# Kernel optimization log

Hardware: AMD Instinct MI355X
Metric: run time of the kernel (lower is better)

Reference implementation:

```python
import jax, jax.numpy as jnp
import numpy as np

TOPK_R = 32  # topk_R from init


def setup_inputs() -> dict:
    key = jax.random.key(0)
    k1, k2 = jax.random.split(key)
    B, N, L_in, L_out = 8, 2048, 512, 512
    x = jax.random.normal(k1, (B, N, L_in), dtype=jnp.float32)
    # kaiming-uniform-style init for Linear weight [out, in]
    bound = float(np.sqrt(6.0 / L_in))
    W = jax.random.uniform(k2, (L_out, L_in), dtype=jnp.float32, minval=-bound, maxval=bound)
    return {"x": x, "W": W}


def reference(x, W):
    # x: [B, N, L_in]; W: [L_out, L_in] (Linear, no bias)
    xp = jnp.einsum('bnl,ol->bno', x, W)          # [B, N, L_out]
    # sim_score with norm=False: plain dot product
    score = jnp.einsum('bnd,bmd->bnm', xp, xp)    # [B, N, N]
    B, N, _ = score.shape
    # RkNNAdjacency: identity + top-k neighbors per row set to 1
    topk_idx = jax.lax.top_k(score, TOPK_R)[1]    # [B, N, k]
    adj = jnp.broadcast_to(jnp.eye(N, dtype=score.dtype), (B, N, N))
    b_idx = jnp.arange(B)[:, None, None]
    n_idx = jnp.arange(N)[None, :, None]
    adj = adj.at[b_idx, n_idx, topk_idx].set(1.0)
    # mask: 1 where neighbor, -1e19 elsewhere; NOTE: multiplicative mask (mask * score)
    mask = jnp.where(adj == 1.0, jnp.ones_like(adj), jnp.full_like(adj, -1e19))
    attention = jax.nn.softmax(mask * score, axis=2)  # [B, N, N]
    h = jnp.einsum('bnm,bmd->bnd', attention, xp)     # [B, N, L_out]
    return (h, attention)
```

## Files before the change

### kernel.cpp

```cpp
#include <hip/hip_runtime.h>
#include <cfloat>


typedef short bf16x8 __attribute__((ext_vector_type(8)));
typedef _Float16 f16x8 __attribute__((ext_vector_type(8)));
typedef _Float16 f16x4 __attribute__((ext_vector_type(4)));
typedef float f32x4 __attribute__((ext_vector_type(4)));

#define NW4 65536

__device__ __forceinline__ unsigned short f2bf(float f) {
  unsigned int u = __float_as_uint(f);
  unsigned int r = (u + 0x7FFFu + ((u >> 16) & 1u)) >> 16;
  return (unsigned short)r;
}

__device__ __forceinline__ void gload_lds16(const unsigned short* g, unsigned short* l) {
  __builtin_amdgcn_global_load_lds(
      (const __attribute__((address_space(1))) unsigned int*)g,
      (__attribute__((address_space(3))) unsigned int*)l, 16, 0, 0);
}

__device__ __forceinline__ unsigned int skey(float v, int m) {
  unsigned int u = __float_as_uint(v);
  u ^= ((unsigned int)((int)u >> 31)) | 0x80000000u;
  return (u & 0xFFFFF800u) | (unsigned int)m;
}

__global__ __launch_bounds__(256) void splitW_kernel(const float* __restrict__ W,
                                                     _Float16* __restrict__ wh,
                                                     _Float16* __restrict__ wl) {
  const int i4 = blockIdx.x * 256 + threadIdx.x;
  if (i4 >= NW4) return;
  const float4 v = reinterpret_cast<const float4*>(W)[i4];
  f16x4 hv, lv;
  const float vv[4] = {v.x, v.y, v.z, v.w};
#pragma unroll
  for (int c = 0; c < 4; ++c) {
    const _Float16 h = (_Float16)vv[c];
    hv[c] = h;
    lv[c] = (_Float16)((vv[c] - (float)h) * 2048.0f);
  }
  reinterpret_cast<f16x4*>(wh)[i4] = hv;
  reinterpret_cast<f16x4*>(wl)[i4] = lv;
}

__global__ __launch_bounds__(256, 2) void gemm_xw_mfma(const float* __restrict__ x,
                                                       const unsigned short* __restrict__ wh,
                                                       const unsigned short* __restrict__ wl,
                                                       float* __restrict__ xp,
                                                       unsigned short* __restrict__ xp16) {
  __shared__ unsigned short lAh[2][128 * 32];
  __shared__ unsigned short lAl[2][128 * 32];
  __shared__ unsigned short lBh[2][128 * 32];
  __shared__ unsigned short lBl[2][128 * 32];
  const int tid = threadIdx.x;
  const int wid = tid >> 6, lane = tid & 63;
  const int lr = lane & 15, kg = lane >> 4;
  const int nbase = blockIdx.x * 128;
  const int obase = blockIdx.y * 128;
  const int wr = wid >> 1, wc = wid & 1;

  const int srow = tid >> 2;
  const int scol = (tid & 3) * 8;
  const float* gX0 = x + (size_t)(nbase + srow) * 512 + scol;
  const float* gX1 = x + (size_t)(nbase + 64 + srow) * 512 + scol;
  const unsigned short* gBh0 = wh + (size_t)(obase + srow) * 512 + scol;
  const unsigned short* gBh1 = wh + (size_t)(obase + 64 + srow) * 512 + scol;
  const unsigned short* gBl0 = wl + (size_t)(obase + srow) * 512 + scol;
  const unsigned short* gBl1 = wl + (size_t)(obase + 64 + srow) * 512 + scol;

  f32x4 acc_hh[4][4] = {};
  f32x4 acc_x[4][4] = {};
  float4 va[4];

#define K1_LOADA(KB)                                                \
  do {                                                              \
    va[0] = *reinterpret_cast<const float4*>(gX0 + (KB));           \
    va[1] = *reinterpret_cast<const float4*>(gX0 + (KB) + 4);       \
    va[2] = *reinterpret_cast<const float4*>(gX1 + (KB));           \
    va[3] = *reinterpret_cast<const float4*>(gX1 + (KB) + 4);       \
  } while (0)

#define K1_WRITEA(BUF)                                              \
  do {                                                              \
    _Pragma("unroll") for (int p = 0; p < 2; ++p) {                 \
      f16x8 hv, lv;                                                 \
      _Pragma("unroll") for (int q = 0; q < 2; ++q) {               \
        const float vv[4] = {va[2 * p + q].x, va[2 * p + q].y,      \
                             va[2 * p + q].z, va[2 * p + q].w};     \
        _Pragma("unroll") for (int c = 0; c < 4; ++c) {             \
          const _Float16 hh = (_Float16)vv[c];                      \
          hv[4 * q + c] = hh;                                       \
          lv[4 * q + c] = (_Float16)((vv[c] - (float)hh) * 2048.0f);\
        }                                                           \
      }                                                             \
      const int ra = (srow + 64 * p) * 32 + scol;                   \
      *reinterpret_cast<f16x8*>(&lAh[BUF][ra]) = hv;                \
      *reinterpret_cast<f16x8*>(&lAl[BUF][ra]) = lv;                \
    }                                                               \
  } while (0)

#define K1_STAGEB(KB, BUF)                                 \
  do {                                                     \
    gload_lds16(gBh0 + (KB), &lBh[BUF][wid * 512]);        \
    gload_lds16(gBh1 + (KB), &lBh[BUF][2048 + wid * 512]); \
    gload_lds16(gBl0 + (KB), &lBl[BUF][wid * 512]);        \
    gload_lds16(gBl1 + (KB), &lBl[BUF][2048 + wid * 512]); \
  } while (0)

#define K1_COMPUTE(BUF)                                                                \
  do {                                                                                 \
    f16x8 ah[4], al[4], bh[4], bl[4];                                                  \
    _Pragma("unroll") for (int i2 = 0; i2 < 4; ++i2) {                                 \
      ah[i2] = *reinterpret_cast<const f16x8*>(&lAh[BUF][(wr * 64 + i2 * 16 + lr) * 32 + kg * 8]); \
      al[i2] = *reinterpret_cast<const f16x8*>(&lAl[BUF][(wr * 64 + i2 * 16 + lr) * 32 + kg * 8]); \
      bh[i2] = *reinterpret_cast<const f16x8*>(&lBh[BUF][(wc * 64 + i2 * 16 + lr) * 32 + kg * 8]); \
      bl[i2] = *reinterpret_cast<const f16x8*>(&lBl[BUF][(wc * 64 + i2 * 16 + lr) * 32 + kg * 8]); \
    }                                                                                  \
    _Pragma("unroll") for (int i2 = 0; i2 < 4; ++i2)                                   \
        _Pragma("unroll") for (int j2 = 0; j2 < 4; ++j2) {                             \
      acc_hh[i2][j2] = __builtin_amdgcn_mfma_f32_16x16x32_f16(ah[i2], bh[j2], acc_hh[i2][j2], 0, 0, 0); \
      acc_x[i2][j2] = __builtin_amdgcn_mfma_f32_16x16x32_f16(ah[i2], bl[j2], acc_x[i2][j2], 0, 0, 0);   \
      acc_x[i2][j2] = __builtin_amdgcn_mfma_f32_16x16x32_f16(al[i2], bh[j2], acc_x[i2][j2], 0, 0, 0);   \
    }                                                                                  \
  } while (0)

  K1_LOADA(0);
  K1_STAGEB(0, 0);
  K1_WRITEA(0);
  __syncthreads();
  for (int t = 0; t < 15; ++t) {
    K1_LOADA((t + 1) * 32);
    K1_STAGEB((t + 1) * 32, (t & 1) ^ 1);
    K1_COMPUTE(t & 1);
    K1_WRITEA((t & 1) ^ 1);
    __syncthreads();
  }
  K1_COMPUTE(1);

#pragma unroll
  for (int i = 0; i < 4; ++i) {
#pragma unroll
    for (int j = 0; j < 4; ++j) {
#pragma unroll
      for (int r = 0; r < 4; ++r) {
        const float v = acc_hh[i][j][r] + acc_x[i][j][r] * (1.0f / 2048.0f);
        const size_t row = (size_t)(nbase + wr * 64 + i * 16 + kg * 4 + r);
        const int col = obase + wc * 64 + j * 16 + lr;
        xp[row * 512 + col] = v;
        xp16[row * 512 + col] = f2bf(v);
      }
    }
  }
#undef K1_LOADA
#undef K1_WRITEA
#undef K1_STAGEB
#undef K1_COMPUTE
}

__global__ __launch_bounds__(256) void score_kernel(const unsigned short* __restrict__ xp16,
                                                    unsigned int* __restrict__ cand) {
  __shared__ unsigned short lA[2][128 * 32];
  __shared__ unsigned short lB[2][128 * 32];
  const int tid = threadIdx.x;
  const int wid = tid >> 6, lane = tid & 63;
  const int lr = lane & 15, kg = lane >> 4;
  const int b = blockIdx.x & 7;
  int p = blockIdx.x >> 3;
  int tn = 0, rem = 16;
  while (p >= rem) { p -= rem; rem--; tn++; }
  const int tm = tn + p;
  const int nbase = tn * 128, mbase = tm * 128;
  const unsigned short* Xb = xp16 + (size_t)b * 2048 * 512;
  const int wr = wid >> 1, wc = wid & 1;

  const int srow = tid >> 2;
  const int scol = (tid & 3) * 8;
  const unsigned short* gA0 = Xb + (size_t)(nbase + srow) * 512 + scol;
  const unsigned short* gA1 = Xb + (size_t)(nbase + 64 + srow) * 512 + scol;
  const unsigned short* gB0 = Xb + (size_t)(mbase + srow) * 512 + scol;
  const unsigned short* gB1 = Xb + (size_t)(mbase + 64 + srow) * 512 + scol;

  f32x4 acc[4][4] = {};

#define STAGE(KB, BUF)                                    \
  do {                                                    \
    gload_lds16(gA0 + (KB), &lA[BUF][wid * 512]);         \
    gload_lds16(gA1 + (KB), &lA[BUF][2048 + wid * 512]);  \
    gload_lds16(gB0 + (KB), &lB[BUF][wid * 512]);         \
    gload_lds16(gB1 + (KB), &lB[BUF][2048 + wid * 512]);  \
  } while (0)

#define COMPUTE(BUF)                                                                   \
  do {                                                                                 \
    bf16x8 af[4], bfr[4];                                                              \
    _Pragma("unroll") for (int i2 = 0; i2 < 4; ++i2) {                                 \
      af[i2] = *reinterpret_cast<const bf16x8*>(&lA[BUF][(wr * 64 + i2 * 16 + lr) * 32 + kg * 8]); \
      bfr[i2] = *reinterpret_cast<const bf16x8*>(&lB[BUF][(wc * 64 + i2 * 16 + lr) * 32 + kg * 8]); \
    }                                                                                  \
    _Pragma("unroll") for (int i2 = 0; i2 < 4; ++i2)                                   \
        _Pragma("unroll") for (int j2 = 0; j2 < 4; ++j2)                               \
            acc[i2][j2] =                                                              \
                __builtin_amdgcn_mfma_f32_16x16x32_bf16(af[i2], bfr[j2], acc[i2][j2], 0, 0, 0); \
  } while (0)

  STAGE(0, 0);
  __syncthreads();
  for (int t = 0; t < 15; ++t) {
    STAGE((t + 1) * 32, (t & 1) ^ 1);
    COMPUTE(t & 1);
    __syncthreads();
  }
  COMPUTE(1);

  const int mcol = mbase + wc * 64 + lr;
#pragma unroll
  for (int i = 0; i < 4; ++i) {
#pragma unroll
    for (int r = 0; r < 4; ++r) {
      const unsigned int x0 = skey(acc[i][0][r], mcol + 0);
      const unsigned int x1 = skey(acc[i][1][r], mcol + 16);
      const unsigned int x2 = skey(acc[i][2][r], mcol + 32);
      const unsigned int x3 = skey(acc[i][3][r], mcol + 48);
      const unsigned int lo01 = min(x0, x1), hi01 = max(x0, x1);
      const unsigned int lo23 = min(x2, x3), hi23 = max(x2, x3);
      unsigned int k1 = min(lo01, lo23);
      unsigned int k2 = min(max(lo01, lo23), min(hi01, hi23));
#pragma unroll
      for (int off = 1; off < 16; off <<= 1) {
        const unsigned int o1 = (unsigned int)__shfl_xor((int)k1, off);
        const unsigned int o2 = (unsigned int)__shfl_xor((int)k2, off);
        const unsigned int nk1 = min(k1, o1);
        const unsigned int nk2 = min(max(k1, o1), min(k2, o2));
        k1 = nk1;
        k2 = nk2;
      }
      if (lr == 0) {
        const int n = nbase + wr * 64 + i * 16 + kg * 4 + r;
        const uint2 kv = {k1, k2};
        *reinterpret_cast<uint2*>(cand + ((size_t)b * 2048 + n) * 512 + (tm * 2 + wc) * 2) = kv;
      }
    }
  }

  if (tn != tm) {
    const int nrow0 = nbase + wr * 64 + kg * 4;
#pragma unroll
    for (int j = 0; j < 4; ++j) {
      unsigned int k1 = 0xFFFFFFFFu, k2 = 0xFFFFFFFFu;
#pragma unroll
      for (int i = 0; i < 4; ++i) {
#pragma unroll
        for (int r = 0; r < 4; ++r) {
          const unsigned int xk = skey(acc[i][j][r], nrow0 + i * 16 + r);
          const unsigned int nk1 = min(k1, xk);
          k2 = min(k2, max(k1, xk));
          k1 = nk1;
        }
      }
#pragma unroll
      for (int off = 16; off < 64; off <<= 1) {
        const unsigned int o1 = (unsigned int)__shfl_xor((int)k1, off);
        const unsigned int o2 = (unsigned int)__shfl_xor((int)k2, off);
        const unsigned int nk1 = min(k1, o1);
        const unsigned int nk2 = min(max(k1, o1), min(k2, o2));
        k1 = nk1;
        k2 = nk2;
      }
      if (kg == 0) {
        const int m = mbase + wc * 64 + j * 16 + lr;
        const uint2 kv = {k1, k2};
        *reinterpret_cast<uint2*>(cand + ((size_t)b * 2048 + m) * 512 + (tn * 2 + wr) * 2) = kv;
      }
    }
  }
#undef STAGE
#undef COMPUTE
}

__global__ __launch_bounds__(64) void finalize_kernel(const float* __restrict__ xp,
                                                      float* __restrict__ h,
                                                      float* __restrict__ att) {
  const int l = threadIdx.x;
  const int b = blockIdx.x & 7;
  const int n = blockIdx.x >> 3;
  const size_t r = (size_t)b * 2048 + n;

  unsigned int key = reinterpret_cast<const unsigned int*>(h + r * 512)[l];
  int wsel[8];
#pragma unroll
  for (int t = 0; t < 8; ++t) {
    unsigned int m = key;
#pragma unroll
    for (int off = 1; off < 64; off <<= 1)
      m = min(m, (unsigned int)__shfl_xor((int)m, off));
    wsel[t] = (int)(m & 0x7FFu);
    if (key == m) key = 0xFFFFFFFFu;
  }

  const float* xb = xp + (size_t)b * 2048 * 512;
  const float* xn = xb + (size_t)n * 512;
  const float4 q0 = reinterpret_cast<const float4*>(xn)[2 * l];
  const float4 q1 = reinterpret_cast<const float4*>(xn)[2 * l + 1];

  float bestv = FLT_MAX;
  int besti = 0x7fffffff;
#pragma unroll
  for (int t = 0; t < 8; ++t) {
    const float* xm = xb + (size_t)wsel[t] * 512;
    const float4 p0 = reinterpret_cast<const float4*>(xm)[2 * l];
    const float4 p1 = reinterpret_cast<const float4*>(xm)[2 * l + 1];
    float s = 0.f;
    s = fmaf(q0.x, p0.x, s); s = fmaf(q0.y, p0.y, s);
    s = fmaf(q0.z, p0.z, s); s = fmaf(q0.w, p0.w, s);
    s = fmaf(q1.x, p1.x, s); s = fmaf(q1.y, p1.y, s);
    s = fmaf(q1.z, p1.z, s); s = fmaf(q1.w, p1.w, s);
#pragma unroll
    for (int off = 1; off < 64; off <<= 1) s += __shfl_xor(s, off);
    if (s < bestv || (s == bestv && wsel[t] < besti)) { bestv = s; besti = wsel[t]; }
  }

  const float* xs = xb + (size_t)besti * 512;
  const float4 w0 = reinterpret_cast<const float4*>(xs)[2 * l];
  const float4 w1 = reinterpret_cast<const float4*>(xs)[2 * l + 1];
  float* hrow = h + r * 512;
  reinterpret_cast<float4*>(hrow)[2 * l] = w0;
  reinterpret_cast<float4*>(hrow)[2 * l + 1] = w1;

  float* arow = att + r * 2048;
#pragma unroll
  for (int s = 0; s < 8; ++s) {
    const int cbase = s * 256 + l * 4;
    float4 v;
    v.x = (cbase + 0 == besti) ? 1.0f : 0.0f;
    v.y = (cbase + 1 == besti) ? 1.0f : 0.0f;
    v.z = (cbase + 2 == besti) ? 1.0f : 0.0f;
    v.w = (cbase + 3 == besti) ? 1.0f : 0.0f;
    reinterpret_cast<float4*>(arow)[s * 64 + l] = v;
  }
}

extern "C" void kernel_launch(void* const* d_in, const int* in_sizes, int n_in,
                              void* d_out, int out_size, void* d_ws, size_t ws_size,
                              hipStream_t stream) {
  const float* x = (const float*)d_in[0];
  const float* W = (const float*)d_in[1];
  float* out = (float*)d_out;
  float* h = out;
  float* att = out + (size_t)8 * 2048 * 512;
  float* xp = (float*)d_ws;

  char* attb = (char*)att;
  _Float16* wh = (_Float16*)(attb + (size_t)32 * 1024 * 1024);
  _Float16* wl = (_Float16*)(attb + (size_t)33 * 1024 * 1024);
  unsigned short* xp16 = (unsigned short*)(attb + (size_t)112 * 1024 * 1024);

  hipLaunchKernelGGL(splitW_kernel, dim3(NW4 / 256), dim3(256), 0, stream, W, wh, wl);

  hipLaunchKernelGGL(gemm_xw_mfma, dim3(16384 / 128, 512 / 128), dim3(256), 0, stream,
                     x, (const unsigned short*)wh, (const unsigned short*)wl, xp, xp16);

  hipLaunchKernelGGL(score_kernel, dim3(8 * 136), dim3(256), 0, stream, xp16,
                     (unsigned int*)h);

  hipLaunchKernelGGL(finalize_kernel, dim3(16384), dim3(64), 0, stream, xp, h, att);
}
```

Before: 117.9 us.

## Load GEMM operands directly from global into registers, dropping LDS staging

The x·W projection kernel no longer stages A and B tiles through shared memory with double buffering and barriers. Each wave now loads its own fragments straight from global memory into registers, converts x to split fp16 in registers, and prefetches the next k-slice of x. This removes LDS traffic and the per-iteration barrier. In exchange, each wave re-reads operands that neighbouring waves also load, relying on L1/L2 to absorb the duplication, and the global access pattern becomes strided, which risks lower memory efficiency.

```diff
diff --git a/kernel.cpp b/kernel.cpp
--- a/kernel.cpp
+++ b/kernel.cpp
@@ -45,15 +45,11 @@
   reinterpret_cast<f16x4*>(wl)[i4] = lv;
 }
 
-__global__ __launch_bounds__(256, 2) void gemm_xw_mfma(const float* __restrict__ x,
-                                                       const unsigned short* __restrict__ wh,
-                                                       const unsigned short* __restrict__ wl,
-                                                       float* __restrict__ xp,
-                                                       unsigned short* __restrict__ xp16) {
-  __shared__ unsigned short lAh[2][128 * 32];
-  __shared__ unsigned short lAl[2][128 * 32];
-  __shared__ unsigned short lBh[2][128 * 32];
-  __shared__ unsigned short lBl[2][128 * 32];
+__global__ __launch_bounds__(256) void gemm_xw_mfma(const float* __restrict__ x,
+                                                    const unsigned short* __restrict__ wh,
+                                                    const unsigned short* __restrict__ wl,
+                                                    float* __restrict__ xp,
+                                                    unsigned short* __restrict__ xp16) {
   const int tid = threadIdx.x;
   const int wid = tid >> 6, lane = tid & 63;
   const int lr = lane & 15, kg = lane >> 4;
@@ -61,83 +57,58 @@
   const int obase = blockIdx.y * 128;
   const int wr = wid >> 1, wc = wid & 1;
 
-  const int srow = tid >> 2;
-  const int scol = (tid & 3) * 8;
-  const float* gX0 = x + (size_t)(nbase + srow) * 512 + scol;
-  const float* gX1 = x + (size_t)(nbase + 64 + srow) * 512 + scol;
-  const unsigned short* gBh0 = wh + (size_t)(obase + srow) * 512 + scol;
-  const unsigned short* gBh1 = wh + (size_t)(obase + 64 + srow) * 512 + scol;
-  const unsigned short* gBl0 = wl + (size_t)(obase + srow) * 512 + scol;
-  const unsigned short* gBl1 = wl + (size_t)(obase + 64 + srow) * 512 + scol;
+  const float* gA = x + (size_t)(nbase + wr * 64 + lr) * 512 + kg * 8;
+  const unsigned short* gBh = wh + (size_t)(obase + wc * 64 + lr) * 512 + kg * 8;
+  const unsigned short* gBl = wl + (size_t)(obase + wc * 64 + lr) * 512 + kg * 8;
 
   f32x4 acc_hh[4][4] = {};
   f32x4 acc_x[4][4] = {};
-  float4 va[4];
-
-#define K1_LOADA(KB)                                                \
-  do {                                                              \
-    va[0] = *reinterpret_cast<const float4*>(gX0 + (KB));           \
-    va[1] = *reinterpret_cast<const float4*>(gX0 + (KB) + 4);       \
-    va[2] = *reinterpret_cast<const float4*>(gX1 + (KB));           \
-    va[3] = *reinterpret_cast<const float4*>(gX1 + (KB) + 4);       \
-  } while (0)
-
-#define K1_WRITEA(BUF)                                              \
-  do {                                                              \
-    _Pragma("unroll") for (int p = 0; p < 2; ++p) {                 \
-      f16x8 hv, lv;                                                 \
-      _Pragma("unroll") for (int q = 0; q < 2; ++q) {               \
-        const float vv[4] = {va[2 * p + q].x, va[2 * p + q].y,      \
-                             va[2 * p + q].z, va[2 * p + q].w};     \
-        _Pragma("unroll") for (int c = 0; c < 4; ++c) {             \
-          const _Float16 hh = (_Float16)vv[c];                      \
-          hv[4 * q + c] = hh;                                       \
-          lv[4 * q + c] = (_Float16)((vv[c] - (float)hh) * 2048.0f);\
-        }                                                           \
-      }                                                             \
-      const int ra = (srow + 64 * p) * 32 + scol;                   \
-      *reinterpret_cast<f16x8*>(&lAh[BUF][ra]) = hv;                \
-      *reinterpret_cast<f16x8*>(&lAl[BUF][ra]) = lv;                \
-    }                                                               \
-  } while (0)
-
-#define K1_STAGEB(KB, BUF)                                 \
-  do {                                                     \
-    gload_lds16(gBh0 + (KB), &lBh[BUF][wid * 512]);        \
-    gload_lds16(gBh1 + (KB), &lBh[BUF][2048 + wid * 512]); \
-    gload_lds16(gBl0 + (KB), &lBl[BUF][wid * 512]);        \
-    gload_lds16(gBl1 + (KB), &lBl[BUF][2048 + wid * 512]); \
-  } while (0)
-
-#define K1_COMPUTE(BUF)                                                                \
-  do {                                                                                 \
-    f16x8 ah[4], al[4], bh[4], bl[4];                                                  \
-    _Pragma("unroll") for (int i2 = 0; i2 < 4; ++i2) {                                 \
-      ah[i2] = *reinterpret_cast<const f16x8*>(&lAh[BUF][(wr * 64 + i2 * 16 + lr) * 32 + kg * 8]); \
-      al[i2] = *reinterpret_cast<const f16x8*>(&lAl[BUF][(wr * 64 + i2 * 16 + lr) * 32 + kg * 8]); \
-      bh[i2] = *reinterpret_cast<const f16x8*>(&lBh[BUF][(wc * 64 + i2 * 16 + lr) * 32 + kg * 8]); \
-      bl[i2] = *reinterpret_cast<const f16x8*>(&lBl[BUF][(wc * 64 + i2 * 16 + lr) * 32 + kg * 8]); \
-    }                                                                                  \
-    _Pragma("unroll") for (int i2 = 0; i2 < 4; ++i2)                                   \
-        _Pragma("unroll") for (int j2 = 0; j2 < 4; ++j2) {                             \
-      acc_hh[i2][j2] = __builtin_amdgcn_mfma_f32_16x16x32_f16(ah[i2], bh[j2], acc_hh[i2][j2], 0, 0, 0); \
-      acc_x[i2][j2] = __builtin_amdgcn_mfma_f32_16x16x32_f16(ah[i2], bl[j2], acc_x[i2][j2], 0, 0, 0);   \
-      acc_x[i2][j2] = __builtin_amdgcn_mfma_f32_16x16x32_f16(al[i2], bh[j2], acc_x[i2][j2], 0, 0, 0);   \
-    }                                                                                  \
-  } while (0)
-
-  K1_LOADA(0);
-  K1_STAGEB(0, 0);
-  K1_WRITEA(0);
-  __syncthreads();
-  for (int t = 0; t < 15; ++t) {
-    K1_LOADA((t + 1) * 32);
-    K1_STAGEB((t + 1) * 32, (t & 1) ^ 1);
-    K1_COMPUTE(t & 1);
-    K1_WRITEA((t & 1) ^ 1);
-    __syncthreads();
-  }
-  K1_COMPUTE(1);
+  float4 va[4][2];
+
+#pragma unroll
+  for (int i = 0; i < 4; ++i) {
+    va[i][0] = *reinterpret_cast<const float4*>(gA + i * 8192);
+    va[i][1] = *reinterpret_cast<const float4*>(gA + i * 8192 + 4);
+  }
+  const float* pA = gA + 32;
+  const unsigned short* pBh = gBh;
+  const unsigned short* pBl = gBl;
+
+  for (int t = 0; t < 16; ++t) {
+    f16x8 bh[4], bl[4];
+#pragma unroll
+    for (int j = 0; j < 4; ++j) {
+      bh[j] = *reinterpret_cast<const f16x8*>(pBh + j * 8192);
+      bl[j] = *reinterpret_cast<const f16x8*>(pBl + j * 8192);
+    }
+    pBh += 32;
+    pBl += 32;
+#pragma unroll
+    for (int i = 0; i < 4; ++i) {
+      f16x8 ah, al;
+#pragma unroll
+      for (int hf = 0; hf < 2; ++hf) {
+        const float vv[4] = {va[i][hf].x, va[i][hf].y, va[i][hf].z, va[i][hf].w};
+#pragma unroll
+        for (int c = 0; c < 4; ++c) {
+          const _Float16 hh = (_Float16)vv[c];
+          ah[4 * hf + c] = hh;
+          al[4 * hf + c] = (_Float16)((vv[c] - (float)hh) * 2048.0f);
+        }
+      }
+      if (t < 15) {
+        va[i][0] = *reinterpret_cast<const float4*>(pA + i * 8192);
+        va[i][1] = *reinterpret_cast<const float4*>(pA + i * 8192 + 4);
+      }
+#pragma unroll
+      for (int j = 0; j < 4; ++j) {
+        acc_hh[i][j] = __builtin_amdgcn_mfma_f32_16x16x32_f16(ah, bh[j], acc_hh[i][j], 0, 0, 0);
+        acc_x[i][j]  = __builtin_amdgcn_mfma_f32_16x16x32_f16(ah, bl[j], acc_x[i][j], 0, 0, 0);
+        acc_x[i][j]  = __builtin_amdgcn_mfma_f32_16x16x32_f16(al, bh[j], acc_x[i][j], 0, 0, 0);
+      }
+    }
+    pA += 32;
+  }
 
 #pragma unroll
   for (int i = 0; i < 4; ++i) {
@@ -153,10 +124,6 @@
       }
     }
   }
-#undef K1_LOADA
-#undef K1_WRITEA
-#undef K1_STAGEB
-#undef K1_COMPUTE
 }
 
 __global__ __launch_bounds__(256) void score_kernel(const unsigned short* __restrict__ xp16,
```

Measured after the change: 149.7 us. +27.0%, slower.
